# Kernel optimization log

Measured on AMD Instinct MI355X. Metric: run time of the kernel, lower is better.

## Reference

```python
import jax, jax.numpy as jnp
import numpy as np

EPS = 1e-5

def layernorm(x, g, b):
    mu = jnp.mean(x, axis=-1, keepdims=True)
    var = jnp.var(x, axis=-1, keepdims=True)
    return (x - mu) * jax.lax.rsqrt(var + EPS) * g + b

DIM = 1024; CTX = 1024; HEADS = 12; DHEAD = 64; INNER = HEADS * DHEAD
B = 4; F = 2048; J = 1024

def setup_inputs() -> dict:
    key = jax.random.key(0)
    ks = jax.random.split(key, 8)
    s = lambda d: 1.0 / np.sqrt(d)
    return {
        "x": jax.random.normal(ks[0], (B, F, DIM), jnp.float32),
        "tab_x": jax.random.normal(ks[1], (B, J, CTX), jnp.float32),
        "tab_g": jnp.ones((CTX,), jnp.float32), "tab_b": jnp.zeros((CTX,), jnp.float32),
        "vid_g": jnp.ones((DIM,), jnp.float32), "vid_b": jnp.zeros((DIM,), jnp.float32),
        "Wq": jax.random.normal(ks[2], (DIM, INNER), jnp.float32) * s(DIM),
        "Wk": jax.random.normal(ks[3], (CTX, INNER), jnp.float32) * s(CTX),
        "Wv": jax.random.normal(ks[4], (CTX, INNER), jnp.float32) * s(CTX),
        "q_g": jnp.ones((INNER,), jnp.float32), "q_b": jnp.zeros((INNER,), jnp.float32),
        "k_g": jnp.ones((INNER,), jnp.float32), "k_b": jnp.zeros((INNER,), jnp.float32),
        "Wo": jax.random.normal(ks[5], (INNER, DIM), jnp.float32) * s(INNER),
        "bo": jnp.zeros((DIM,), jnp.float32),
    }

def reference(x, tab_x, tab_g, tab_b, vid_g, vid_b, Wq, Wk, Wv, q_g, q_b, k_g, k_b, Wo, bo):
    scale = DHEAD ** -0.5
    kv_in = layernorm(tab_x, tab_g, tab_b)                      # [b,j,ctx]
    q = layernorm(layernorm(x, vid_g, vid_b) @ Wq, q_g, q_b)    # [b,f,inner]
    k = layernorm(kv_in @ Wk, k_g, k_b)                         # [b,j,inner]
    v = kv_in @ Wv                                              # [b,j,inner]
    split = lambda t: t.reshape(t.shape[0], t.shape[1], HEADS, DHEAD).transpose(0, 2, 1, 3)
    q, k, v = split(q) * scale, split(k), split(v)              # [b,h,*,d]
    sim = jnp.einsum('bhid,bhjd->bhij', q, k)
    attn = jax.nn.softmax(sim, axis=-1)
    out = jnp.einsum('bhij,bhjd->bhid', attn, v)                # [b,h,f,d]
    out = out.transpose(0, 2, 1, 3).reshape(x.shape[0], x.shape[1], INNER)
    return out @ Wo + bo
```

## Files before the change

kernel.cpp:

```cpp
#include <hip/hip_runtime.h>

typedef unsigned short u16;
typedef float  f32x4   __attribute__((ext_vector_type(4)));
typedef float  f32x16  __attribute__((ext_vector_type(16)));
typedef __bf16 bf16x8  __attribute__((ext_vector_type(8)));
typedef u16    u16x4   __attribute__((ext_vector_type(4)));

#define DEV __device__ __forceinline__

DEV u16 f2bf(float f) {
  union { float f; unsigned u; } x; x.f = f;
  unsigned r = x.u + 0x7fffu + ((x.u >> 16) & 1u);
  return (u16)(r >> 16);
}
DEV float bf2f(u16 b) { union { unsigned u; float f; } c; c.u = (unsigned)b << 16; return c.f; }

DEV unsigned cvtpk(float lo, float hi) {
  unsigned r;
  asm("v_cvt_pk_bf16_f32 %0, %1, %2" : "=v"(r) : "v"(lo), "v"(hi));
  return r;
}
DEV float fexp2(float x) { return __builtin_exp2f(x); }

DEV f32x4 mfma16(bf16x8 a, bf16x8 b, f32x4 c) {
  return __builtin_amdgcn_mfma_f32_16x16x32_bf16(a, b, c, 0, 0, 0);
}
DEV f32x16 mfma32(bf16x8 a, bf16x8 b, f32x16 c) {
  return __builtin_amdgcn_mfma_f32_32x32x16_bf16(a, b, c, 0, 0, 0);
}

DEV void gload16(const void* g, void* l) {
  __builtin_amdgcn_global_load_lds(
      (__attribute__((address_space(1))) void*)g,
      (__attribute__((address_space(3))) void*)l, 16, 0, 0);
}

template<typename LOADER>
DEV void ln_body(LOADER load, const float* __restrict__ g, const float* __restrict__ bta,
                 u16* __restrict__ yrow, int C, float outscale, float* red)
{
  const int tid = threadIdx.x;
  const int n4 = C >> 2;
  f32x4 v = {0.f, 0.f, 0.f, 0.f};
  if (tid < n4) v = load(tid);
  float s1 = v[0] + v[1] + v[2] + v[3];
  float s2 = v[0]*v[0] + v[1]*v[1] + v[2]*v[2] + v[3]*v[3];
#pragma unroll
  for (int o = 32; o > 0; o >>= 1) {
    s1 += __shfl_xor(s1, o, 64);
    s2 += __shfl_xor(s2, o, 64);
  }
  const int lane = tid & 63, wv = tid >> 6;
  if (lane == 0) { red[wv] = s1; red[4 + wv] = s2; }
  __syncthreads();
  s1 = red[0] + red[1] + red[2] + red[3];
  s2 = red[4] + red[5] + red[6] + red[7];
  const float mu = s1 / C;
  const float rs = rsqrtf(s2 / C - mu * mu + 1e-5f);
  if (tid < n4) {
    f32x4 gg = *(const f32x4*)(g + 4 * tid);
    f32x4 bb = *(const f32x4*)(bta + 4 * tid);
    u16x4 o4;
#pragma unroll
    for (int j = 0; j < 4; ++j)
      o4[j] = f2bf(((v[j] - mu) * rs * gg[j] + bb[j]) * outscale);
    *(u16x4*)(yrow + 4 * tid) = o4;
  }
}

__global__ __launch_bounds__(256)
void prep(const float* __restrict__ Wq, const float* __restrict__ Wk,
          const float* __restrict__ Wv, const float* __restrict__ Wo,
          u16* __restrict__ WqT, u16* __restrict__ WkvT, u16* __restrict__ WoT,
          const float* __restrict__ tabx, const float* __restrict__ tab_g,
          const float* __restrict__ tab_b,
          const float* __restrict__ x, const float* __restrict__ vid_g,
          const float* __restrict__ vid_b,
          u16* __restrict__ kvn, u16* __restrict__ xn)
{
  __shared__ float t[32][33];
  __shared__ float red[8];
  const int bid = blockIdx.x;
  const int tid = threadIdx.x;
  if (bid < 3840) {
    const float* src; u16* dst; int K, N, k0, n0;
    if (bid < 3072) {
      const int w = bid / 768, r = bid % 768;
      src = (w == 0) ? Wq : (w == 1) ? Wk : Wv;
      dst = (w == 0) ? WqT : (w == 1) ? WkvT : WkvT + (size_t)768 * 1024;
      K = 1024; N = 768; k0 = (r % 32) * 32; n0 = (r / 32) * 32;
    } else {
      const int r = bid - 3072;
      src = Wo; dst = WoT;
      K = 768; N = 1024; k0 = (r % 24) * 32; n0 = (r / 24) * 32;
    }
    const int tx = tid & 31, ty = tid >> 5;
#pragma unroll
    for (int i = ty; i < 32; i += 8)
      t[i][tx] = src[(size_t)(k0 + i) * N + n0 + tx];
    __syncthreads();
#pragma unroll
    for (int i = ty; i < 32; i += 8)
      dst[(size_t)(n0 + i) * K + k0 + tx] = f2bf(t[tx][i]);
  } else {
    const int r = bid - 3840;
    const float* xr; const float *g, *bb; u16* y;
    if (r < 4096) { xr = tabx + (size_t)r * 1024; g = tab_g; bb = tab_b;
                    y = kvn + (size_t)r * 1024; }
    else { const int rr = r - 4096; xr = x + (size_t)rr * 1024; g = vid_g;
           bb = vid_b; y = xn + (size_t)rr * 1024; }
    ln_body([&](int i) { return *(const f32x4*)(xr + 4 * i); }, g, bb, y, 1024, 1.0f, red);
  }
}

__global__ __launch_bounds__(256)
void gemm_qkv(const u16* __restrict__ xn, const u16* __restrict__ kvn,
              const u16* __restrict__ WqT, const u16* __restrict__ WkvT,
              u16* __restrict__ q_pre, u16* __restrict__ k_pre, u16* __restrict__ vT)
{
  __shared__ __align__(16) u16 As[2][64 * 64];
  __shared__ __align__(16) u16 Bs[2][128 * 64];
  const int bid = blockIdx.x;
  const int tid  = threadIdx.x;
  const int lane = tid & 63;
  const int wave = tid >> 6;
  const bool isq = bid >= 768;
  const u16* A; const u16* Bt; int bm, bn;
  if (!isq) { A = kvn;  Bt = WkvT; bm = (bid & 63) * 64;  bn = (bid >> 6) * 128; }
  else { const int r = bid - 768; A = xn; Bt = WqT; bm = (r & 127) * 64; bn = (r >> 7) * 128; }
  const int wm = (wave >> 1) * 32;
  const int wn = (wave & 1) * 64;
  const int fr = lane & 15;
  const int fkb = (lane >> 4) * 16;

  f32x4 acc[2][4] = {};
  const char* gA0 = (const char*)(A  + (size_t)bm * 1024);
  const char* gB0 = (const char*)(Bt + (size_t)bn * 1024);
  const size_t rowpitch = 2048;

  auto stage = [&](int buf, int k0) {
#pragma unroll
    for (int c = 0; c < 2; ++c) {
      const int off = tid * 16 + c * 4096;
      const int row = off >> 7;
      const int scol = (off & 127) ^ ((row & 7) << 4);
      gload16(gA0 + (size_t)row * rowpitch + 2 * k0 + scol,
              (char*)&As[buf][0] + wave * 1024 + c * 4096);
    }
#pragma unroll
    for (int c = 0; c < 4; ++c) {
      const int off = tid * 16 + c * 4096;
      const int row = off >> 7;
      const int scol = (off & 127) ^ ((row & 7) << 4);
      gload16(gB0 + (size_t)row * rowpitch + 2 * k0 + scol,
              (char*)&Bs[buf][0] + wave * 1024 + c * 4096);
    }
  };

  auto step = [&](int cur) {
    bf16x8 af[2][2], bg[4][2];
#pragma unroll
    for (int m = 0; m < 2; ++m)
#pragma unroll
      for (int kk = 0; kk < 2; ++kk) {
        const int row = wm + m * 16 + fr;
        af[m][kk] = *(const bf16x8*)((const char*)&As[cur][0] + row * 128 +
                                     ((kk * 64 + fkb) ^ ((row & 7) << 4)));
      }
#pragma unroll
    for (int n = 0; n < 4; ++n)
#pragma unroll
      for (int kk = 0; kk < 2; ++kk) {
        const int row = wn + n * 16 + fr;
        bg[n][kk] = *(const bf16x8*)((const char*)&Bs[cur][0] + row * 128 +
                                     ((kk * 64 + fkb) ^ ((row & 7) << 4)));
      }
#pragma unroll
    for (int kk = 0; kk < 2; ++kk)
#pragma unroll
      for (int m = 0; m < 2; ++m)
#pragma unroll
        for (int n = 0; n < 4; ++n)
          acc[m][n] = mfma16(af[m][kk], bg[n][kk], acc[m][n]);
  };

  stage(0, 0);
#pragma unroll 1
  for (int t = 0; t < 15; ++t) {
    stage((t & 1) ^ 1, (t + 1) * 64);
    asm volatile("s_waitcnt vmcnt(6)" ::: "memory");
    __builtin_amdgcn_s_barrier();
    step(t & 1);
    __builtin_amdgcn_s_barrier();
    asm volatile("" ::: "memory");
  }
  asm volatile("s_waitcnt vmcnt(0)" ::: "memory");
  __builtin_amdgcn_s_barrier();
  step(15 & 1);

  const int orow0 = bm + wm + 4 * (lane >> 4);
  const int ocol0 = bn + wn + fr;
#pragma unroll
  for (int m = 0; m < 2; ++m)
#pragma unroll
    for (int n = 0; n < 4; ++n) {
      const int row0 = orow0 + m * 16;
      const int col  = ocol0 + n * 16;
      if (isq) {
#pragma unroll
        for (int r = 0; r < 4; ++r)
          q_pre[(size_t)(row0 + r) * 768 + col] = f2bf(acc[m][n][r]);
      } else if (bn < 768) {
#pragma unroll
        for (int r = 0; r < 4; ++r)
          k_pre[(size_t)(row0 + r) * 768 + col] = f2bf(acc[m][n][r]);
      } else {
        const int c2 = col - 768, hh = c2 >> 6, dd = c2 & 63;
        const int bb2 = row0 >> 10, jj = row0 & 1023;
        u16x4 o4;
#pragma unroll
        for (int r = 0; r < 4; ++r) o4[r] = f2bf(acc[m][n][r]);
        *(u16x4*)(vT + ((size_t)(bb2 * 12 + hh) * 64 + dd) * 1024 + jj) = o4;
      }
    }
}

__global__ __launch_bounds__(256)
void ln_qk(const u16* __restrict__ k_pre, const float* __restrict__ k_g,
           const float* __restrict__ k_b, u16* __restrict__ kb,
           const u16* __restrict__ q_pre, const float* __restrict__ q_g,
           const float* __restrict__ q_b, u16* __restrict__ qb)
{
  __shared__ float red[8];
  const int bid = blockIdx.x;
  const bool isk = bid < 4096;
  const int row = isk ? bid : bid - 4096;
  const u16* xr = (isk ? k_pre : q_pre) + (size_t)row * 768;
  u16* y = (isk ? kb : qb) + (size_t)row * 768;
  const float sc = isk ? 1.0f : 0.125f * 1.44269504089f;
  ln_body([&](int i) {
    const u16x4 raw = *(const u16x4*)(xr + 4 * i);
    f32x4 v;
#pragma unroll
    for (int j = 0; j < 4; ++j) v[j] = bf2f(raw[j]);
    return v;
  }, isk ? k_g : q_g, isk ? k_b : q_b, y, 768, sc, red);
}

__global__ __launch_bounds__(256, 3)
void attn7(const u16* __restrict__ q, const u16* __restrict__ k,
           const u16* __restrict__ vT, u16* __restrict__ att)
{
  __shared__ __align__(16) u16 Ks[2][64 * 64];
  __shared__ __align__(16) u16 Vs[2][64 * 64];
  __shared__ __align__(16) u16 osm[4][32][72];

  const int bh = blockIdx.x;
  const int b = bh / 12, h = bh - b * 12;
  const int tid = threadIdx.x, lane = tid & 63, wave = tid >> 6;
  const int lq  = lane & 31;
  const int hi5 = lane >> 5;
  const int qrow = blockIdx.y * 128 + wave * 32 + lq;

  const u16* qp = q + (size_t)(b * 2048 + qrow) * 768 + h * 64 + hi5 * 8;
  bf16x8 qf[4];
#pragma unroll
  for (int ds = 0; ds < 4; ++ds) qf[ds] = *(const bf16x8*)(qp + ds * 16);

  f32x16 ot0 = {}, ot1 = {};
  float l0 = 0.f, l1 = 0.f, l2 = 0.f, l3 = 0.f;

  const char* kg = (const char*)k + (size_t)(b * 1024) * 1536 + h * 128;
  const char* vg = (const char*)vT + (size_t)bh * 64 * 2048;
  const int rsw0 = (lq & 7) << 4;

  auto stage = [&](int buf, int j0) {
#pragma unroll
    for (int c = 0; c < 2; ++c) {
      const int o   = tid * 16 + c * 4096;
      const int row = o >> 7;
      const int scol = (o & 127) ^ ((row & 7) << 4);
      gload16(kg + (size_t)(j0 + row) * 1536 + scol,
              (char*)&Ks[buf][0] + wave * 1024 + c * 4096);
      gload16(vg + (size_t)row * 2048 + (size_t)j0 * 2 + scol,
              (char*)&Vs[buf][0] + wave * 1024 + c * 4096);
    }
  };

  auto step = [&](int cur) {
    f32x16 st0 = {}, st1 = {};
    __builtin_amdgcn_s_setprio(1);
#pragma unroll
    for (int ds = 0; ds < 4; ++ds) {
      const int cb = ds * 32 + hi5 * 16;
      const bf16x8 k0 = *(const bf16x8*)((const char*)&Ks[cur][0] + lq * 128 + (cb ^ rsw0));
      const bf16x8 k1 = *(const bf16x8*)((const char*)&Ks[cur][0] + (lq + 32) * 128 + (cb ^ rsw0));
      st0 = mfma32(k0, qf[ds], st0);
      st1 = mfma32(k1, qf[ds], st1);
    }
    __builtin_amdgcn_s_setprio(0);
#pragma unroll
    for (int r = 0; r < 16; r += 4) {
      float p0 = fexp2(st0[r]);     st0[r]     = p0; l0 += p0;
      float p1 = fexp2(st0[r + 1]); st0[r + 1] = p1; l1 += p1;
      float p2 = fexp2(st0[r + 2]); st0[r + 2] = p2; l2 += p2;
      float p3 = fexp2(st0[r + 3]); st0[r + 3] = p3; l3 += p3;
    }
#pragma unroll
    for (int r = 0; r < 16; r += 4) {
      float p0 = fexp2(st1[r]);     st1[r]     = p0; l0 += p0;
      float p1 = fexp2(st1[r + 1]); st1[r + 1] = p1; l1 += p1;
      float p2 = fexp2(st1[r + 2]); st1[r + 2] = p2; l2 += p2;
      float p3 = fexp2(st1[r + 3]); st1[r + 3] = p3; l3 += p3;
    }
    __builtin_amdgcn_s_setprio(1);
#pragma unroll
    for (int s4 = 0; s4 < 4; ++s4) {
      const int u = (s4 & 1) * 8;
      float a0, a1, a2, a3, b0, b1, b2, b3;
      if (s4 < 2) {
        a0 = st0[u]; a1 = st0[u + 1]; a2 = st0[u + 2]; a3 = st0[u + 3];
        b0 = st0[u + 4]; b1 = st0[u + 5]; b2 = st0[u + 6]; b3 = st0[u + 7];
      } else {
        a0 = st1[u]; a1 = st1[u + 1]; a2 = st1[u + 2]; a3 = st1[u + 3];
        b0 = st1[u + 4]; b1 = st1[u + 5]; b2 = st1[u + 6]; b3 = st1[u + 7];
      }
      const unsigned L0 = cvtpk(a0, a1), L1 = cvtpk(a2, a3);
      const unsigned H0 = cvtpk(b0, b1), H1 = cvtpk(b2, b3);
      const auto w02 = __builtin_amdgcn_permlane32_swap(L0, H0, false, false);
      const auto w13 = __builtin_amdgcn_permlane32_swap(L1, H1, false, false);
      union BU { unsigned w[4]; bf16x8 v; } pu;
      pu.w[0] = w02[0]; pu.w[1] = w13[0]; pu.w[2] = w02[1]; pu.w[3] = w13[1];
      const int cb = s4 * 32 + hi5 * 16;
      const bf16x8 v0 = *(const bf16x8*)((const char*)&Vs[cur][0] + lq * 128 + (cb ^ rsw0));
      const bf16x8 v1 = *(const bf16x8*)((const char*)&Vs[cur][0] + (lq + 32) * 128 + (cb ^ rsw0));
      ot0 = mfma32(v0, pu.v, ot0);
      ot1 = mfma32(v1, pu.v, ot1);
    }
    __builtin_amdgcn_s_setprio(0);
  };

  stage(0, 0);
#pragma unroll 1
  for (int tt = 0; tt < 7; ++tt) {
    stage(1, (2 * tt + 1) * 64);
    asm volatile("s_waitcnt vmcnt(4)" ::: "memory");
    __builtin_amdgcn_s_barrier();
    step(0);
    __builtin_amdgcn_s_barrier();
    stage(0, (2 * tt + 2) * 64);
    asm volatile("s_waitcnt vmcnt(4)" ::: "memory");
    __builtin_amdgcn_s_barrier();
    step(1);
    __builtin_amdgcn_s_barrier();
    asm volatile("" ::: "memory");
  }
  stage(1, 15 * 64);
  asm volatile("s_waitcnt vmcnt(4)" ::: "memory");
  __builtin_amdgcn_s_barrier();
  step(0);
  __builtin_amdgcn_s_barrier();
  asm volatile("s_waitcnt vmcnt(0)" ::: "memory");
  __builtin_amdgcn_s_barrier();
  step(1);

  float l = (l0 + l1) + (l2 + l3);
  l += __shfl_xor(l, 32, 64);
  const float inv = 1.0f / l;
#pragma unroll
  for (int r = 0; r < 16; ++r) {
    const int d0 = (r & 3) + 8 * (r >> 2) + 4 * hi5;
    osm[wave][lq][d0]      = f2bf(ot0[r] * inv);
    osm[wave][lq][32 + d0] = f2bf(ot1[r] * inv);
  }
  asm volatile("s_waitcnt lgkmcnt(0)" ::: "memory");
  const int col = (lane & 7) * 8;
#pragma unroll
  for (int pass = 0; pass < 4; ++pass) {
    const int row = pass * 8 + (lane >> 3);
    const bf16x8 vv = *(const bf16x8*)&osm[wave][row][col];
    const int qg = blockIdx.y * 128 + wave * 32 + row;
    *(bf16x8*)(att + (size_t)(b * 2048 + qg) * 768 + h * 64 + col) = vv;
  }
}

__global__ __launch_bounds__(256)
void gemm_o(const u16* __restrict__ A, const u16* __restrict__ Bt,
            float* __restrict__ Cp, const float* __restrict__ bias)
{
  __shared__ __align__(16) u16 As[2][64 * 64];
  __shared__ __align__(16) u16 Bs[2][128 * 64];
  const int tid  = threadIdx.x;
  const int lane = tid & 63;
  const int wave = tid >> 6;
  const int bm = blockIdx.x * 64;
  const int bn = blockIdx.y * 128;
  const int wm = (wave >> 1) * 32;
  const int wn = (wave & 1) * 64;
  const int fr = lane & 15;
  const int fkb = (lane >> 4) * 16;

  f32x4 acc[2][4] = {};
  const char* gA0 = (const char*)(A  + (size_t)bm * 768);
  const char* gB0 = (const char*)(Bt + (size_t)bn * 768);
  const size_t rowpitch = 1536;

  auto stage = [&](int buf, int k0) {
#pragma unroll
    for (int c = 0; c < 2; ++c) {
      const int off = tid * 16 + c * 4096;
      const int row = off >> 7;
      const int scol = (off & 127) ^ ((row & 7) << 4);
      gload16(gA0 + (size_t)row * rowpitch + 2 * k0 + scol,
              (char*)&As[buf][0] + wave * 1024 + c * 4096);
    }
#pragma unroll
    for (int c = 0; c < 4; ++c) {
      const int off = tid * 16 + c * 4096;
      const int row = off >> 7;
      const int scol = (off & 127) ^ ((row & 7) << 4);
      gload16(gB0 + (size_t)row * rowpitch + 2 * k0 + scol,
              (char*)&Bs[buf][0] + wave * 1024 + c * 4096);
    }
  };

  auto step = [&](int cur) {
    bf16x8 af[2][2], bg[4][2];
#pragma unroll
    for (int m = 0; m < 2; ++m)
#pragma unroll
      for (int kk = 0; kk < 2; ++kk) {
        const int row = wm + m * 16 + fr;
        af[m][kk] = *(const bf16x8*)((const char*)&As[cur][0] + row * 128 +
                                     ((kk * 64 + fkb) ^ ((row & 7) << 4)));
      }
#pragma unroll
    for (int n = 0; n < 4; ++n)
#pragma unroll
      for (int kk = 0; kk < 2; ++kk) {
        const int row = wn + n * 16 + fr;
        bg[n][kk] = *(const bf16x8*)((const char*)&Bs[cur][0] + row * 128 +
                                     ((kk * 64 + fkb) ^ ((row & 7) << 4)));
      }
#pragma unroll
    for (int kk = 0; kk < 2; ++kk)
#pragma unroll
      for (int m = 0; m < 2; ++m)
#pragma unroll
        for (int n = 0; n < 4; ++n)
          acc[m][n] = mfma16(af[m][kk], bg[n][kk], acc[m][n]);
  };

  stage(0, 0);
#pragma unroll 1
  for (int t = 0; t < 11; ++t) {
    stage((t & 1) ^ 1, (t + 1) * 64);
    asm volatile("s_waitcnt vmcnt(6)" ::: "memory");
    __builtin_amdgcn_s_barrier();
    step(t & 1);
    __builtin_amdgcn_s_barrier();
    asm volatile("" ::: "memory");
  }
  asm volatile("s_waitcnt vmcnt(0)" ::: "memory");
  __builtin_amdgcn_s_barrier();
  step(11 & 1);

  const int orow0 = bm + wm + 4 * (lane >> 4);
  const int ocol0 = bn + wn + fr;
#pragma unroll
  for (int m = 0; m < 2; ++m)
#pragma unroll
    for (int n = 0; n < 4; ++n)
#pragma unroll
      for (int r = 0; r < 4; ++r) {
        const int row = orow0 + m * 16 + r;
        const int col = ocol0 + n * 16;
        Cp[(size_t)row * 1024 + col] = acc[m][n][r] + bias[col];
      }
}

extern "C" void kernel_launch(void* const* d_in, const int* in_sizes, int n_in,
                              void* d_out, int out_size, void* d_ws, size_t ws_size,
                              hipStream_t stream)
{
  const float* x     = (const float*)d_in[0];
  const float* tabx  = (const float*)d_in[1];
  const float* tab_g = (const float*)d_in[2];
  const float* tab_b = (const float*)d_in[3];
  const float* vid_g = (const float*)d_in[4];
  const float* vid_b = (const float*)d_in[5];
  const float* Wq    = (const float*)d_in[6];
  const float* Wk    = (const float*)d_in[7];
  const float* Wv    = (const float*)d_in[8];
  const float* q_g   = (const float*)d_in[9];
  const float* q_b   = (const float*)d_in[10];
  const float* k_g   = (const float*)d_in[11];
  const float* k_b   = (const float*)d_in[12];
  const float* Wo    = (const float*)d_in[13];
  const float* bo    = (const float*)d_in[14];

  char* ws = (char*)d_ws;
  const size_t O_WQT  = 0;
  const size_t O_WKVT = O_WQT  + (size_t)768 * 1024 * 2;
  const size_t O_WOT  = O_WKVT + (size_t)1536 * 1024 * 2;
  const size_t O_XN   = O_WOT  + (size_t)1024 * 768 * 2;
  const size_t O_KVN  = O_XN   + (size_t)8192 * 1024 * 2;
  const size_t O_QPRE = O_KVN  + (size_t)4096 * 1024 * 2;
  const size_t O_KPRE = O_QPRE + (size_t)8192 * 768 * 2;
  const size_t O_QB   = O_KPRE + (size_t)4096 * 768 * 2;
  const size_t O_KB   = O_QB   + (size_t)8192 * 768 * 2;
  const size_t O_VT   = O_KB   + (size_t)4096 * 768 * 2;
  const size_t O_ATT  = O_QPRE;

  u16*   WqT   = (u16*)(ws + O_WQT);
  u16*   WkvT  = (u16*)(ws + O_WKVT);
  u16*   WoT   = (u16*)(ws + O_WOT);
  u16*   xn    = (u16*)(ws + O_XN);
  u16*   kvn   = (u16*)(ws + O_KVN);
  u16*   q_pre = (u16*)(ws + O_QPRE);
  u16*   k_pre = (u16*)(ws + O_KPRE);
  u16*   qb    = (u16*)(ws + O_QB);
  u16*   kb    = (u16*)(ws + O_KB);
  u16*   vT    = (u16*)(ws + O_VT);
  u16*   attb  = (u16*)(ws + O_ATT);

  prep<<<16128, 256, 0, stream>>>(Wq, Wk, Wv, Wo, WqT, WkvT, WoT,
                                  tabx, tab_g, tab_b, x, vid_g, vid_b, kvn, xn);
  gemm_qkv<<<1536, 256, 0, stream>>>(xn, kvn, WqT, WkvT, q_pre, k_pre, vT);
  ln_qk<<<12288, 256, 0, stream>>>(k_pre, k_g, k_b, kb, q_pre, q_g, q_b, qb);
  attn7<<<dim3(48, 16), 256, 0, stream>>>(qb, kb, vT, attb);
  gemm_o<<<dim3(128, 8), 256, 0, stream>>>(attb, WoT, (float*)d_out, bo);
}
```

Measured before the change: 134.7 us.

## Use 128x128x32 tiles in QKV and output GEMMs, hardware exp2

Both GEMM kernels move from 64x128 tiles with K-step 64 to 128x128 tiles with K-step 32. Each wave now computes a 64x64 sub-tile, which doubles MFMA work per LDS fragment load and halves the number of blocks. The shared-memory swizzle and the staging are reworked for 64-byte rows. The exp2 helper also switches to the hardware builtin when it is available. The cost is more accumulator registers, half as many workgroups, and twice as many barriered k-iterations.

```diff
diff --git a/kernel.cpp b/kernel.cpp
--- a/kernel.cpp
+++ b/kernel.cpp
@@ -20,7 +20,11 @@
   asm("v_cvt_pk_bf16_f32 %0, %1, %2" : "=v"(r) : "v"(lo), "v"(hi));
   return r;
 }
+#if __has_builtin(__builtin_amdgcn_exp2f)
+DEV float fexp2(float x) { return __builtin_amdgcn_exp2f(x); }
+#else
 DEV float fexp2(float x) { return __builtin_exp2f(x); }
+#endif
 
 DEV f32x4 mfma16(bf16x8 a, bf16x8 b, f32x4 c) {
   return __builtin_amdgcn_mfma_f32_16x16x32_bf16(a, b, c, 0, 0, 0);
@@ -118,22 +122,22 @@
               const u16* __restrict__ WqT, const u16* __restrict__ WkvT,
               u16* __restrict__ q_pre, u16* __restrict__ k_pre, u16* __restrict__ vT)
 {
-  __shared__ __align__(16) u16 As[2][64 * 64];
-  __shared__ __align__(16) u16 Bs[2][128 * 64];
+  __shared__ __align__(16) u16 As[2][128 * 32];
+  __shared__ __align__(16) u16 Bs[2][128 * 32];
   const int bid = blockIdx.x;
   const int tid  = threadIdx.x;
   const int lane = tid & 63;
   const int wave = tid >> 6;
-  const bool isq = bid >= 768;
+  const bool isq = bid >= 384;
   const u16* A; const u16* Bt; int bm, bn;
-  if (!isq) { A = kvn;  Bt = WkvT; bm = (bid & 63) * 64;  bn = (bid >> 6) * 128; }
-  else { const int r = bid - 768; A = xn; Bt = WqT; bm = (r & 127) * 64; bn = (r >> 7) * 128; }
-  const int wm = (wave >> 1) * 32;
+  if (!isq) { A = kvn;  Bt = WkvT; bm = (bid & 31) * 128;  bn = (bid >> 5) * 128; }
+  else { const int r = bid - 384; A = xn; Bt = WqT; bm = (r & 63) * 128; bn = (r >> 6) * 128; }
+  const int wm = (wave >> 1) * 64;
   const int wn = (wave & 1) * 64;
   const int fr = lane & 15;
   const int fkb = (lane >> 4) * 16;
 
-  f32x4 acc[2][4] = {};
+  f32x4 acc[4][4] = {};
   const char* gA0 = (const char*)(A  + (size_t)bm * 1024);
   const char* gB0 = (const char*)(Bt + (size_t)bn * 1024);
   const size_t rowpitch = 2048;
@@ -142,53 +146,41 @@
 #pragma unroll
     for (int c = 0; c < 2; ++c) {
       const int off = tid * 16 + c * 4096;
-      const int row = off >> 7;
-      const int scol = (off & 127) ^ ((row & 7) << 4);
+      const int row = off >> 6;
+      const int scol = (off & 63) ^ ((row & 3) << 4);
       gload16(gA0 + (size_t)row * rowpitch + 2 * k0 + scol,
               (char*)&As[buf][0] + wave * 1024 + c * 4096);
-    }
-#pragma unroll
-    for (int c = 0; c < 4; ++c) {
-      const int off = tid * 16 + c * 4096;
-      const int row = off >> 7;
-      const int scol = (off & 127) ^ ((row & 7) << 4);
       gload16(gB0 + (size_t)row * rowpitch + 2 * k0 + scol,
               (char*)&Bs[buf][0] + wave * 1024 + c * 4096);
     }
   };
 
   auto step = [&](int cur) {
-    bf16x8 af[2][2], bg[4][2];
-#pragma unroll
-    for (int m = 0; m < 2; ++m)
-#pragma unroll
-      for (int kk = 0; kk < 2; ++kk) {
-        const int row = wm + m * 16 + fr;
-        af[m][kk] = *(const bf16x8*)((const char*)&As[cur][0] + row * 128 +
-                                     ((kk * 64 + fkb) ^ ((row & 7) << 4)));
-      }
-#pragma unroll
-    for (int n = 0; n < 4; ++n)
-#pragma unroll
-      for (int kk = 0; kk < 2; ++kk) {
-        const int row = wn + n * 16 + fr;
-        bg[n][kk] = *(const bf16x8*)((const char*)&Bs[cur][0] + row * 128 +
-                                     ((kk * 64 + fkb) ^ ((row & 7) << 4)));
-      }
-#pragma unroll
-    for (int kk = 0; kk < 2; ++kk)
-#pragma unroll
-      for (int m = 0; m < 2; ++m)
-#pragma unroll
-        for (int n = 0; n < 4; ++n)
-          acc[m][n] = mfma16(af[m][kk], bg[n][kk], acc[m][n]);
+    bf16x8 af[4], bg[4];
+#pragma unroll
+    for (int m = 0; m < 4; ++m) {
+      const int row = wm + m * 16 + fr;
+      af[m] = *(const bf16x8*)((const char*)&As[cur][0] + row * 64 +
+                               (fkb ^ ((row & 3) << 4)));
+    }
+#pragma unroll
+    for (int n = 0; n < 4; ++n) {
+      const int row = wn + n * 16 + fr;
+      bg[n] = *(const bf16x8*)((const char*)&Bs[cur][0] + row * 64 +
+                               (fkb ^ ((row & 3) << 4)));
+    }
+#pragma unroll
+    for (int m = 0; m < 4; ++m)
+#pragma unroll
+      for (int n = 0; n < 4; ++n)
+        acc[m][n] = mfma16(af[m], bg[n], acc[m][n]);
   };
 
   stage(0, 0);
 #pragma unroll 1
-  for (int t = 0; t < 15; ++t) {
-    stage((t & 1) ^ 1, (t + 1) * 64);
-    asm volatile("s_waitcnt vmcnt(6)" ::: "memory");
+  for (int t = 0; t < 31; ++t) {
+    stage((t & 1) ^ 1, (t + 1) * 32);
+    asm volatile("s_waitcnt vmcnt(4)" ::: "memory");
     __builtin_amdgcn_s_barrier();
     step(t & 1);
     __builtin_amdgcn_s_barrier();
@@ -196,12 +188,12 @@
   }
   asm volatile("s_waitcnt vmcnt(0)" ::: "memory");
   __builtin_amdgcn_s_barrier();
-  step(15 & 1);
+  step(31 & 1);
 
   const int orow0 = bm + wm + 4 * (lane >> 4);
   const int ocol0 = bn + wn + fr;
 #pragma unroll
-  for (int m = 0; m < 2; ++m)
+  for (int m = 0; m < 4; ++m)
 #pragma unroll
     for (int n = 0; n < 4; ++n) {
       const int row0 = orow0 + m * 16;
@@ -210,7 +202,7 @@
 #pragma unroll
         for (int r = 0; r < 4; ++r)
           q_pre[(size_t)(row0 + r) * 768 + col] = f2bf(acc[m][n][r]);
-      } else if (bn < 768) {
+      } else if (col < 768) {
 #pragma unroll
         for (int r = 0; r < 4; ++r)
           k_pre[(size_t)(row0 + r) * 768 + col] = f2bf(acc[m][n][r]);
@@ -388,19 +380,19 @@
 void gemm_o(const u16* __restrict__ A, const u16* __restrict__ Bt,
             float* __restrict__ Cp, const float* __restrict__ bias)
 {
-  __shared__ __align__(16) u16 As[2][64 * 64];
-  __shared__ __align__(16) u16 Bs[2][128 * 64];
+  __shared__ __align__(16) u16 As[2][128 * 32];
+  __shared__ __align__(16) u16 Bs[2][128 * 32];
   const int tid  = threadIdx.x;
   const int lane = tid & 63;
   const int wave = tid >> 6;
-  const int bm = blockIdx.x * 64;
+  const int bm = blockIdx.x * 128;
   const int bn = blockIdx.y * 128;
-  const int wm = (wave >> 1) * 32;
+  const int wm = (wave >> 1) * 64;
   const int wn = (wave & 1) * 64;
   const int fr = lane & 15;
   const int fkb = (lane >> 4) * 16;
 
-  f32x4 acc[2][4] = {};
+  f32x4 acc[4][4] = {};
   const char* gA0 = (const char*)(A  + (size_t)bm * 768);
   const char* gB0 = (const char*)(Bt + (size_t)bn * 768);
   const size_t rowpitch = 1536;
@@ -409,53 +401,41 @@
 #pragma unroll
     for (int c = 0; c < 2; ++c) {
       const int off = tid * 16 + c * 4096;
-      const int row = off >> 7;
-      const int scol = (off & 127) ^ ((row & 7) << 4);
+      const int row = off >> 6;
+      const int scol = (off & 63) ^ ((row & 3) << 4);
       gload16(gA0 + (size_t)row * rowpitch + 2 * k0 + scol,
               (char*)&As[buf][0] + wave * 1024 + c * 4096);
-    }
-#pragma unroll
-    for (int c = 0; c < 4; ++c) {
-      const int off = tid * 16 + c * 4096;
-      const int row = off >> 7;
-      const int scol = (off & 127) ^ ((row & 7) << 4);
       gload16(gB0 + (size_t)row * rowpitch + 2 * k0 + scol,
               (char*)&Bs[buf][0] + wave * 1024 + c * 4096);
     }
   };
 
   auto step = [&](int cur) {
-    bf16x8 af[2][2], bg[4][2];
-#pragma unroll
-    for (int m = 0; m < 2; ++m)
-#pragma unroll
-      for (int kk = 0; kk < 2; ++kk) {
-        const int row = wm + m * 16 + fr;
-        af[m][kk] = *(const bf16x8*)((const char*)&As[cur][0] + row * 128 +
-                                     ((kk * 64 + fkb) ^ ((row & 7) << 4)));
-      }
-#pragma unroll
-    for (int n = 0; n < 4; ++n)
-#pragma unroll
-      for (int kk = 0; kk < 2; ++kk) {
-        const int row = wn + n * 16 + fr;
-        bg[n][kk] = *(const bf16x8*)((const char*)&Bs[cur][0] + row * 128 +
-                                     ((kk * 64 + fkb) ^ ((row & 7) << 4)));
-      }
-#pragma unroll
-    for (int kk = 0; kk < 2; ++kk)
-#pragma unroll
-      for (int m = 0; m < 2; ++m)
-#pragma unroll
-        for (int n = 0; n < 4; ++n)
-          acc[m][n] = mfma16(af[m][kk], bg[n][kk], acc[m][n]);
+    bf16x8 af[4], bg[4];
+#pragma unroll
+    for (int m = 0; m < 4; ++m) {
+      const int row = wm + m * 16 + fr;
+      af[m] = *(const bf16x8*)((const char*)&As[cur][0] + row * 64 +
+                               (fkb ^ ((row & 3) << 4)));
+    }
+#pragma unroll
+    for (int n = 0; n < 4; ++n) {
+      const int row = wn + n * 16 + fr;
+      bg[n] = *(const bf16x8*)((const char*)&Bs[cur][0] + row * 64 +
+                               (fkb ^ ((row & 3) << 4)));
+    }
+#pragma unroll
+    for (int m = 0; m < 4; ++m)
+#pragma unroll
+      for (int n = 0; n < 4; ++n)
+        acc[m][n] = mfma16(af[m], bg[n], acc[m][n]);
   };
 
   stage(0, 0);
 #pragma unroll 1
-  for (int t = 0; t < 11; ++t) {
-    stage((t & 1) ^ 1, (t + 1) * 64);
-    asm volatile("s_waitcnt vmcnt(6)" ::: "memory");
+  for (int t = 0; t < 23; ++t) {
+    stage((t & 1) ^ 1, (t + 1) * 32);
+    asm volatile("s_waitcnt vmcnt(4)" ::: "memory");
     __builtin_amdgcn_s_barrier();
     step(t & 1);
     __builtin_amdgcn_s_barrier();
@@ -463,12 +443,12 @@
   }
   asm volatile("s_waitcnt vmcnt(0)" ::: "memory");
   __builtin_amdgcn_s_barrier();
-  step(11 & 1);
+  step(23 & 1);
 
   const int orow0 = bm + wm + 4 * (lane >> 4);
   const int ocol0 = bn + wn + fr;
 #pragma unroll
-  for (int m = 0; m < 2; ++m)
+  for (int m = 0; m < 4; ++m)
 #pragma unroll
     for (int n = 0; n < 4; ++n)
 #pragma unroll
@@ -526,8 +506,8 @@
 
   prep<<<16128, 256, 0, stream>>>(Wq, Wk, Wv, Wo, WqT, WkvT, WoT,
                                   tabx, tab_g, tab_b, x, vid_g, vid_b, kvn, xn);
-  gemm_qkv<<<1536, 256, 0, stream>>>(xn, kvn, WqT, WkvT, q_pre, k_pre, vT);
+  gemm_qkv<<<768, 256, 0, stream>>>(xn, kvn, WqT, WkvT, q_pre, k_pre, vT);
   ln_qk<<<12288, 256, 0, stream>>>(k_pre, k_g, k_b, kb, q_pre, q_g, q_b, qb);
   attn7<<<dim3(48, 16), 256, 0, stream>>>(qb, kb, vT, attb);
-  gemm_o<<<dim3(128, 8), 256, 0, stream>>>(attb, WoT, (float*)d_out, bo);
-}
+  gemm_o<<<dim3(64, 8), 256, 0, stream>>>(attb, WoT, (float*)d_out, bo);
+}
```

After: 129.0 us. 1.04x faster.
